# Optimization experiments

Measured on AMD Instinct MI355X. Metric: run time of the kernel, lower is better.

## Reference

```python
import jax, jax.numpy as jnp
import numpy as np

D = 256; FF = 1024; NH = 8; NL = 4; NP = 4; DH = D // NH
SHAPES = [(64, 64), (32, 32), (16, 16), (8, 8)]
B = 4; N = sum(h * w for h, w in SHAPES)


def _ln(x, g, b, eps=1e-5):
    m = jnp.mean(x, -1, keepdims=True)
    v = jnp.var(x, -1, keepdims=True)
    return (x - m) * jax.lax.rsqrt(v + eps) * g + b


def _bilinear(v, x, y, H, W):
    # v: [B, H*W, nh, dh]; x, y: [B, Nq, nh, P] pixel coords (grid_sample, align_corners=False, zero pad)
    x0 = jnp.floor(x); y0 = jnp.floor(y)
    fx = x - x0; fy = y - y0
    x0 = x0.astype(jnp.int32); y0 = y0.astype(jnp.int32)
    dh = v.shape[-1]
    acc = 0.0
    for xi, yi, w in ((x0, y0, (1 - fx) * (1 - fy)),
                      (x0 + 1, y0, fx * (1 - fy)),
                      (x0, y0 + 1, (1 - fx) * fy),
                      (x0 + 1, y0 + 1, fx * fy)):
        valid = ((xi >= 0) & (xi < W) & (yi >= 0) & (yi < H)).astype(v.dtype)
        idx = jnp.clip(yi, 0, H - 1) * W + jnp.clip(xi, 0, W - 1)  # [B,Nq,nh,P]
        Bq, Nq, nh, P = idx.shape
        idx2 = idx.transpose(0, 1, 3, 2).reshape(Bq, Nq * P, nh, 1)
        idx2 = jnp.broadcast_to(idx2, (Bq, Nq * P, nh, dh))
        g = jnp.take_along_axis(v, idx2, axis=1)  # [B, Nq*P, nh, dh]
        g = g.reshape(Bq, Nq, P, nh, dh).transpose(0, 1, 3, 2, 4)  # [B,Nq,nh,P,dh]
        acc = acc + g * (w * valid)[..., None]
    return acc


def _msdeform(value, loc, attn, shapes):
    # value [B,N,nh,dh]; loc [B,Nq,nh,L,P,2] in [0,1]; attn [B,Nq,nh,L,P]
    out = 0.0; start = 0
    for l, (H, W) in enumerate(shapes):
        v = value[:, start:start + H * W]
        start += H * W
        x = loc[:, :, :, l, :, 0] * W - 0.5
        y = loc[:, :, :, l, :, 1] * H - 0.5
        s = _bilinear(v, x, y, H, W)  # [B,Nq,nh,P,dh]
        out = out + jnp.einsum('bqhpd,bqhp->bqhd', s, attn[:, :, :, l, :])
    return out


def _forward(src, pos, reference_points, w_value, b_value, w_off, b_off, w_attn, b_attn,
             w_out, b_out, g1, be1, w1, b1, w2, b2, g2, be2, padding_mask, shapes):
    q = src + pos
    value = src @ w_value.T + b_value
    value = jnp.where(padding_mask[..., None], 0.0, value).reshape(B, N, NH, DH)
    off = (q @ w_off.T + b_off).reshape(B, N, NH, NL, NP, 2)
    attn = jax.nn.softmax((q @ w_attn.T + b_attn).reshape(B, N, NH, NL * NP), axis=-1)
    attn = attn.reshape(B, N, NH, NL, NP)
    normalizer = jnp.array([[w, h] for h, w in shapes], jnp.float32)  # [L,2] as (W,H)
    loc = reference_points[:, :, None, :, None, :] + off / normalizer[None, None, None, :, None, :]
    a = _msdeform(value, loc, attn, shapes).reshape(B, N, D) @ w_out.T + b_out
    x = _ln(src + a, g1, be1)
    f = jax.nn.relu(x @ w1.T + b1) @ w2.T + b2
    return _ln(x + f, g2, be2)


def setup_inputs() -> dict:
    key = jax.random.key(0)
    ks = iter(jax.random.split(key, 24))
    def p(shape, scale=0.02):
        return jax.random.normal(next(ks), shape, jnp.float32) * scale
    d = {}
    d['src'] = jax.random.normal(next(ks), (B, N, D), jnp.float32)
    d['pos'] = jax.random.normal(next(ks), (B, N, D), jnp.float32)
    d['reference_points'] = jax.random.uniform(next(ks), (B, N, NL, 2), dtype=jnp.float32)
    d['w_value'] = p((D, D)); d['b_value'] = jnp.zeros((D,), jnp.float32)
    d['w_off'] = p((NH * NL * NP * 2, D), 0.001); d['b_off'] = p((NH * NL * NP * 2,), 0.1)
    d['w_attn'] = p((NH * NL * NP, D)); d['b_attn'] = jnp.zeros((NH * NL * NP,), jnp.float32)
    d['w_out'] = p((D, D)); d['b_out'] = jnp.zeros((D,), jnp.float32)
    d['g1'] = jnp.ones((D,), jnp.float32); d['be1'] = jnp.zeros((D,), jnp.float32)
    d['w1'] = p((FF, D)); d['b1'] = jnp.zeros((FF,), jnp.float32)
    d['w2'] = p((D, FF)); d['b2'] = jnp.zeros((D,), jnp.float32)
    d['g2'] = jnp.ones((D,), jnp.float32); d['be2'] = jnp.zeros((D,), jnp.float32)
    d['spatial_shapes'] = jnp.array(SHAPES, jnp.int32)
    d['level_start_index'] = jnp.array(np.cumsum([0] + [h * w for h, w in SHAPES[:-1]]), jnp.int32)
    d['padding_mask'] = jnp.zeros((B, N), bool)
    return d


def reference(src, pos, reference_points, w_value, b_value, w_off, b_off, w_attn, b_attn,
              w_out, b_out, g1, be1, w1, b1, w2, b2, g2, be2,
              spatial_shapes, level_start_index, padding_mask):
    shapes = [tuple(map(int, s)) for s in np.asarray(spatial_shapes)]  # static per-level shapes
    return _forward(src, pos, reference_points, w_value, b_value, w_off, b_off, w_attn, b_attn,
                    w_out, b_out, g1, be1, w1, b1, w2, b2, g2, be2, padding_mask, shapes)
```

## Files before the change

### kernel.cpp

```cpp
#include <hip/hip_runtime.h>

#define B_SZ   4
#define NTOK   5440
#define MTOT   (B_SZ*NTOK)
#define DMODEL 256
#define FFDIM  1024

typedef __attribute__((ext_vector_type(8))) __bf16 bf16x8;
typedef __attribute__((ext_vector_type(4))) float  f32x4;

static __device__ __forceinline__ unsigned short f2b(float f) {
    unsigned u = __builtin_bit_cast(unsigned, f);
    u = (u + 0x7FFF + ((u >> 16) & 1)) >> 16;
    return (unsigned short)u;
}
static __device__ __forceinline__ float b2f(unsigned short s) {
    return __builtin_bit_cast(float, (unsigned)s << 16);
}
static __device__ __forceinline__ float lo_bf(unsigned u) {
    return __builtin_bit_cast(float, u << 16);
}
static __device__ __forceinline__ float hi_bf(unsigned u) {
    return __builtin_bit_cast(float, u & 0xffff0000u);
}

__global__ __launch_bounds__(256)
void mfma_gemm(const unsigned short* __restrict__ A,
               const unsigned short* __restrict__ Wt,
               const float* __restrict__ bias, const float* __restrict__ bias2,
               int bsplit,
               const unsigned char* __restrict__ rowmask,
               float* __restrict__ Cf, unsigned short* __restrict__ Cb,
               int M, int Nout, int K, int relu)
{
    __shared__ unsigned short As[128 * 32];
    __shared__ unsigned short Bs[128 * 32];
    const int tid  = threadIdx.x;
    const int lane = tid & 63;
    const int wave = tid >> 6;
    const int row0 = blockIdx.x * 128, col0 = blockIdx.y * 128;
    const int wr = (wave >> 1) * 64;
    const int wc = (wave & 1) * 64;
    const int mrow = lane & 15, quad = lane >> 4;

    f32x4 acc[4][4] = {};

    const int r0i = (0 * 256 + tid) >> 2, k0i = ((0 * 256 + tid) & 3) * 8;
    const int r1i = (1 * 256 + tid) >> 2, k1i = ((1 * 256 + tid) & 3) * 8;
    const int lds0 = (0 * 256 + wave * 64) * 8;
    const int lds1 = (1 * 256 + wave * 64) * 8;

    for (int k0 = 0; k0 < K; k0 += 32) {
        __syncthreads();
        {
            const unsigned short* ga0 = A  + (size_t)(row0 + r0i) * K + k0 + k0i;
            const unsigned short* gb0 = Wt + (size_t)(col0 + r0i) * K + k0 + k0i;
            const unsigned short* ga1 = A  + (size_t)(row0 + r1i) * K + k0 + k1i;
            const unsigned short* gb1 = Wt + (size_t)(col0 + r1i) * K + k0 + k1i;
            __builtin_amdgcn_global_load_lds((const __attribute__((address_space(1))) void*)ga0,
                                             (__attribute__((address_space(3))) void*)&As[lds0], 16, 0, 0);
            __builtin_amdgcn_global_load_lds((const __attribute__((address_space(1))) void*)gb0,
                                             (__attribute__((address_space(3))) void*)&Bs[lds0], 16, 0, 0);
            __builtin_amdgcn_global_load_lds((const __attribute__((address_space(1))) void*)ga1,
                                             (__attribute__((address_space(3))) void*)&As[lds1], 16, 0, 0);
            __builtin_amdgcn_global_load_lds((const __attribute__((address_space(1))) void*)gb1,
                                             (__attribute__((address_space(3))) void*)&Bs[lds1], 16, 0, 0);
        }
        __syncthreads();

        bf16x8 af[4], bfr[4];
        #pragma unroll
        for (int t4 = 0; t4 < 4; ++t4) {
            af[t4]  = *(const bf16x8*)&As[(wr + t4 * 16 + mrow) * 32 + quad * 8];
            bfr[t4] = *(const bf16x8*)&Bs[(wc + t4 * 16 + mrow) * 32 + quad * 8];
        }
        #pragma unroll
        for (int ti = 0; ti < 4; ++ti)
            #pragma unroll
            for (int tj = 0; tj < 4; ++tj)
                acc[ti][tj] = __builtin_amdgcn_mfma_f32_16x16x32_bf16(
                                  af[ti], bfr[tj], acc[ti][tj], 0, 0, 0);
    }

    #pragma unroll
    for (int tj = 0; tj < 4; ++tj) {
        const int col = col0 + wc + tj * 16 + mrow;
        const float bv = (col < bsplit) ? bias[col] : bias2[col - bsplit];
        #pragma unroll
        for (int ti = 0; ti < 4; ++ti) {
            #pragma unroll
            for (int r = 0; r < 4; ++r) {
                const int row = row0 + wr + ti * 16 + quad * 4 + r;
                float v = acc[ti][tj][r] + bv;
                if (relu) v = fmaxf(v, 0.f);
                if (rowmask && rowmask[row]) v = 0.f;
                if (Cf) Cf[(size_t)row * Nout + col] = v;
                else    Cb[(size_t)row * Nout + col] = f2b(v);
            }
        }
    }
}

__global__ __launch_bounds__(256)
void sampling_kernel(const unsigned short* __restrict__ value,
                     const unsigned short* __restrict__ oa,
                     const float* __restrict__ refp,
                     unsigned short* __restrict__ samp)
{
    __shared__ int4 s_pk[1024];
    const int t0  = blockIdx.x * 4;
    const int tid = threadIdx.x;

    #pragma unroll
    for (int rep = 0; rep < 2; ++rep) {
        const int e   = rep * 256 + tid;
        const int tok = e >> 7;
        const int hp  = e & 127;
        const int h   = hp >> 4, i16 = hp & 15, l = i16 >> 2;
        const int t   = t0 + tok;

        const float logit = b2f(oa[(size_t)t * 384 + 256 + h * 16 + i16]);
        float mx = logit;
        #pragma unroll
        for (int o = 8; o; o >>= 1) mx = fmaxf(mx, __shfl_xor(mx, o, 16));
        const float ex = __expf(logit - mx);
        float ssum = ex;
        #pragma unroll
        for (int o = 8; o; o >>= 1) ssum += __shfl_xor(ssum, o, 16);
        const float aw = ex / ssum;

        const int   Wl_t[4]   = {64, 32, 16, 8};
        const int   LSTB_t[4] = {0, 4096 * 512, 5120 * 512, 5376 * 512};
        const int   Wl   = Wl_t[l];
        const int   LSTB = LSTB_t[l];
        const float fW   = (float)Wl;

        const unsigned ov = *(const unsigned*)&oa[(size_t)t * 384 + h * 32 + i16 * 2];
        const float ox = lo_bf(ov), oy = hi_bf(ov);
        const float2 rxy = *(const float2*)&refp[(size_t)t * 8 + l * 2];
        const float x = rxy.x * fW + ox - 0.5f;
        const float y = rxy.y * fW + oy - 0.5f;
        const float x0 = floorf(x), y0 = floorf(y);
        const float fx = x - x0, fy = y - y0;
        const int   ix = (int)x0, iy = (int)y0;
        const bool  vx0 = (ix >= 0) & (ix < Wl), vx1 = (ix + 1 >= 0) & (ix + 1 < Wl);

        #pragma unroll
        for (int j = 0; j < 2; ++j) {
            const int  yv = iy + j;
            const bool vy = (yv >= 0) & (yv < Wl);
            const float wy = (j ? fy : 1.f - fy) * aw;
            const int  rowb = LSTB + yv * Wl * 512;
            const float w0 = (vy & vx0) ? wy * (1.f - fx) : 0.f;
            const float w1 = (vy & vx1) ? wy * fx : 0.f;
            const int  i0 = (vy & vx0) ? rowb + ix * 512 : 0;
            const int  i1 = (vy & vx1) ? rowb + (ix + 1) * 512 : 0;
            s_pk[e * 2 + j] = make_int4(i0, __float_as_int(w0), i1, __float_as_int(w1));
        }
    }
    __syncthreads();

    const int wv_  = tid >> 6;
    const int lane = tid & 63;
    const int h    = lane >> 3, dq = lane & 7;
    const int t    = t0 + wv_;
    const int b    = t / NTOK;
    const char* vb = (const char*)value + ((size_t)b * NTOK * 256 + h * 32 + dq * 4) * 2;
    const int4* pk = s_pk + (wv_ * 128 + h * 16) * 2;

    float a0 = 0.f, a1 = 0.f, a2 = 0.f, a3 = 0.f;
    #pragma unroll 8
    for (int i = 0; i < 32; ++i) {
        const int4 p = pk[i];
        const uint2 u0 = *(const uint2*)(vb + p.x);
        const uint2 u1 = *(const uint2*)(vb + p.z);
        const float w0 = __int_as_float(p.y), w1 = __int_as_float(p.w);
        a0 += lo_bf(u0.x) * w0; a1 += hi_bf(u0.x) * w0;
        a2 += lo_bf(u0.y) * w0; a3 += hi_bf(u0.y) * w0;
        a0 += lo_bf(u1.x) * w1; a1 += hi_bf(u1.x) * w1;
        a2 += lo_bf(u1.y) * w1; a3 += hi_bf(u1.y) * w1;
    }
    ushort4 o;
    o.x = f2b(a0); o.y = f2b(a1); o.z = f2b(a2); o.w = f2b(a3);
    *(ushort4*)(samp + (size_t)t * 256 + h * 32 + dq * 4) = o;
}

__global__ __launch_bounds__(256)
void ln_kernel(const float* __restrict__ resid, const float* __restrict__ y,
               const float* __restrict__ g, const float* __restrict__ be,
               float* __restrict__ out_f, unsigned short* __restrict__ out_b)
{
    const int wave = threadIdx.x >> 6;
    const int lane = threadIdx.x & 63;
    const int row  = blockIdx.x * 4 + wave;
    const size_t base = (size_t)row * 256 + (lane << 2);

    const float4 r = *(const float4*)(resid + base);
    float4 v       = *(const float4*)(y + base);
    v.x += r.x; v.y += r.y; v.z += r.z; v.w += r.w;

    float s  = v.x + v.y + v.z + v.w;
    float ss = v.x * v.x + v.y * v.y + v.z * v.z + v.w * v.w;
    #pragma unroll
    for (int off = 32; off; off >>= 1) {
        s  += __shfl_xor(s, off, 64);
        ss += __shfl_xor(ss, off, 64);
    }
    const float mean = s * (1.f / 256.f);
    const float var  = ss * (1.f / 256.f) - mean * mean;
    const float rstd = rsqrtf(var + 1e-5f);

    const float4 gv = *(const float4*)(g  + (lane << 2));
    const float4 bv = *(const float4*)(be + (lane << 2));
    float4 o;
    o.x = (v.x - mean) * rstd * gv.x + bv.x;
    o.y = (v.y - mean) * rstd * gv.y + bv.y;
    o.z = (v.z - mean) * rstd * gv.z + bv.z;
    o.w = (v.w - mean) * rstd * gv.w + bv.w;
    *(float4*)(out_f + base) = o;
    if (out_b) {
        ushort4 u; u.x = f2b(o.x); u.y = f2b(o.y); u.z = f2b(o.z); u.w = f2b(o.w);
        *(ushort4*)(out_b + base) = u;
    }
}

__global__ __launch_bounds__(256)
void prep_kernel(const float* __restrict__ src, const float* __restrict__ pos,
                 const float* __restrict__ wv, const float* __restrict__ woff,
                 const float* __restrict__ wattn, const float* __restrict__ wout,
                 const float* __restrict__ w1, const float* __restrict__ w2,
                 unsigned short* __restrict__ q_bf, unsigned short* __restrict__ src_bf,
                 unsigned short* __restrict__ wv_b, unsigned short* __restrict__ woa_b,
                 unsigned short* __restrict__ wout_b,
                 unsigned short* __restrict__ w1_b, unsigned short* __restrict__ w2_b)
{
    const int v = blockIdx.x * 256 + threadIdx.x;
    if (v < 1392640) {
        const float4 s = ((const float4*)src)[v];
        const float4 p = ((const float4*)pos)[v];
        ushort4 qo, so;
        qo.x = f2b(s.x + p.x); qo.y = f2b(s.y + p.y);
        qo.z = f2b(s.z + p.z); qo.w = f2b(s.w + p.w);
        so.x = f2b(s.x); so.y = f2b(s.y); so.z = f2b(s.z); so.w = f2b(s.w);
        ((ushort4*)q_bf)[v]   = qo;
        ((ushort4*)src_bf)[v] = so;
        return;
    }
    const int v2 = v - 1392640;
    const float* s; unsigned short* d; int off;
    if      (v2 <  16384) { s = wv;    d = wv_b;          off = v2; }
    else if (v2 <  32768) { s = woff;  d = woa_b;         off = v2 - 16384; }
    else if (v2 <  40960) { s = wattn; d = woa_b + 65536; off = v2 - 32768; }
    else if (v2 <  57344) { s = wout;  d = wout_b;        off = v2 - 40960; }
    else if (v2 < 122880) { s = w1;    d = w1_b;          off = v2 - 57344; }
    else                  { s = w2;    d = w2_b;          off = v2 - 122880; }
    const float4 f = ((const float4*)s)[off];
    ushort4 u; u.x = f2b(f.x); u.y = f2b(f.y); u.z = f2b(f.z); u.w = f2b(f.w);
    ((ushort4*)d)[off] = u;
}

extern "C" void kernel_launch(void* const* d_in, const int* in_sizes, int n_in,
                              void* d_out, int out_size, void* d_ws, size_t ws_size,
                              hipStream_t stream) {
    const float* src     = (const float*)d_in[0];
    const float* pos     = (const float*)d_in[1];
    const float* refp    = (const float*)d_in[2];
    const float* w_value = (const float*)d_in[3];
    const float* b_value = (const float*)d_in[4];
    const float* w_off   = (const float*)d_in[5];
    const float* b_off   = (const float*)d_in[6];
    const float* w_attn  = (const float*)d_in[7];
    const float* b_attn  = (const float*)d_in[8];
    const float* w_out   = (const float*)d_in[9];
    const float* b_out   = (const float*)d_in[10];
    const float* g1      = (const float*)d_in[11];
    const float* be1     = (const float*)d_in[12];
    const float* w1      = (const float*)d_in[13];
    const float* b1      = (const float*)d_in[14];
    const float* w2      = (const float*)d_in[15];
    const float* b2      = (const float*)d_in[16];
    const float* g2      = (const float*)d_in[17];
    const float* be2     = (const float*)d_in[18];
    const unsigned char* pmask = (const unsigned char*)d_in[21];

    char* ws = (char*)d_ws;
    const size_t SZ16 = (size_t)MTOT * 256 * 2;
    unsigned short* q_bf    = (unsigned short*)(ws);
    unsigned short* src_bf  = (unsigned short*)(ws + SZ16);
    float*          aout    = (float*)(ws);
    float*          f       = (float*)(ws);
    unsigned short* value_b = (unsigned short*)(ws + 2 * SZ16);
    unsigned short* oa_b    = (unsigned short*)(ws + 3 * SZ16);
    float*          x       = (float*)(ws + 2 * SZ16);
    unsigned short* samp    = (unsigned short*)(ws + 50135040ULL);
    unsigned short* x_bf    = (unsigned short*)(ws + 50135040ULL);
    unsigned short* h_bf    = (unsigned short*)(ws + 61276160ULL);
    unsigned short* wts     = (unsigned short*)(ws + 105840640ULL);
    unsigned short* wv_b    = wts;
    unsigned short* woa_b   = wv_b   + 65536;
    unsigned short* wout_b  = woa_b  + 98304;
    unsigned short* w1_b    = wout_b + 65536;
    unsigned short* w2_b    = w1_b   + 262144;

    const dim3 blk(256);

    prep_kernel<<<dim3(6176), blk, 0, stream>>>(src, pos, w_value, w_off, w_attn,
                                                w_out, w1, w2, q_bf, src_bf,
                                                wv_b, woa_b, wout_b, w1_b, w2_b);
    mfma_gemm<<<dim3(MTOT / 128, 2), blk, 0, stream>>>(
        src_bf, wv_b, b_value, b_value, DMODEL, pmask, nullptr, value_b,
        MTOT, DMODEL, DMODEL, 0);
    mfma_gemm<<<dim3(MTOT / 128, 3), blk, 0, stream>>>(
        q_bf, woa_b, b_off, b_attn, DMODEL, nullptr, nullptr, oa_b,
        MTOT, 384, DMODEL, 0);
    sampling_kernel<<<dim3(MTOT / 4), blk, 0, stream>>>(value_b, oa_b, refp, samp);
    mfma_gemm<<<dim3(MTOT / 128, 2), blk, 0, stream>>>(
        samp, wout_b, b_out, b_out, DMODEL, nullptr, aout, nullptr,
        MTOT, DMODEL, DMODEL, 0);
    ln_kernel<<<dim3(MTOT / 4), blk, 0, stream>>>(src, aout, g1, be1, x, x_bf);
    mfma_gemm<<<dim3(MTOT / 128, FFDIM / 128), blk, 0, stream>>>(
        x_bf, w1_b, b1, b1, FFDIM, nullptr, nullptr, h_bf, MTOT, FFDIM, DMODEL, 1);
    mfma_gemm<<<dim3(MTOT / 128, 2), blk, 0, stream>>>(
        h_bf, w2_b, b2, b2, DMODEL, nullptr, f, nullptr, MTOT, DMODEL, FFDIM, 0);
    ln_kernel<<<dim3(MTOT / 4), blk, 0, stream>>>(x, f, g2, be2, (float*)d_out, nullptr);
}
```

Measured before the change: 318.9 us.

## Fuse value/offset GEMMs, fuse LayerNorm into output GEMMs, pad sampling LDS

The separate value and offset/attention projection GEMMs are merged into a single launch that chooses its operands per block column. The output-projection and FFN2 GEMMs now use full-row 64x256 tiles and apply bias, residual add and LayerNorm in the epilogue, which removes both standalone LN kernels and the fp32 intermediate round trips. The sampling kernel's shared-memory packet array is padded to a stride of 33 per head to reduce bank conflicts. The workspace layout is rearranged to match. The trade-off is that the LN-fused GEMMs launch fewer, taller blocks (340) and each block loads the whole 256-column weight slice.

```diff
diff --git a/kernel.cpp b/kernel.cpp
--- a/kernel.cpp
+++ b/kernel.cpp
@@ -24,13 +24,86 @@
     return __builtin_bit_cast(float, u & 0xffff0000u);
 }
 
+#define GLL(gp, lp) __builtin_amdgcn_global_load_lds( \
+    (const __attribute__((address_space(1))) void*)(gp), \
+    (__attribute__((address_space(3))) void*)(lp), 16, 0, 0)
+
+__global__ __launch_bounds__(256)
+void qkv_gemm(const unsigned short* __restrict__ src_bf,
+              const unsigned short* __restrict__ q_bf,
+              const unsigned short* __restrict__ wv_b,
+              const unsigned short* __restrict__ woa_b,
+              const float* __restrict__ b_value,
+              const float* __restrict__ b_off, const float* __restrict__ b_attn,
+              const unsigned char* __restrict__ rowmask,
+              unsigned short* __restrict__ value_b, unsigned short* __restrict__ oa_b)
+{
+    const int K = 256;
+    const int y = blockIdx.y;
+    const bool isv = (y < 2);
+    const unsigned short* A  = isv ? src_bf : q_bf;
+    const unsigned short* Wt = isv ? wv_b : woa_b;
+    unsigned short* C = isv ? value_b : oa_b;
+    const int ldc  = isv ? 256 : 384;
+    const int col0 = (isv ? y : (y - 2)) * 128;
+
+    __shared__ unsigned short As[128 * 32];
+    __shared__ unsigned short Bs[128 * 32];
+    const int tid  = threadIdx.x;
+    const int lane = tid & 63;
+    const int wave = tid >> 6;
+    const int row0 = blockIdx.x * 128;
+    const int wr = (wave >> 1) * 64, wc = (wave & 1) * 64;
+    const int mrow = lane & 15, quad = lane >> 4;
+
+    f32x4 acc[4][4] = {};
+    const int ri0 = tid >> 2,            ki0 = (tid & 3) * 8;
+    const int ri1 = (256 + tid) >> 2,    ki1 = ((256 + tid) & 3) * 8;
+    const int lds0 = (wave * 64) * 8, lds1 = (256 + wave * 64) * 8;
+
+    for (int k0 = 0; k0 < K; k0 += 32) {
+        __syncthreads();
+        GLL(A  + (size_t)(row0 + ri0) * K + k0 + ki0, &As[lds0]);
+        GLL(Wt + (size_t)(col0 + ri0) * K + k0 + ki0, &Bs[lds0]);
+        GLL(A  + (size_t)(row0 + ri1) * K + k0 + ki1, &As[lds1]);
+        GLL(Wt + (size_t)(col0 + ri1) * K + k0 + ki1, &Bs[lds1]);
+        __syncthreads();
+
+        bf16x8 af[4], bfr[4];
+        #pragma unroll
+        for (int t4 = 0; t4 < 4; ++t4) {
+            af[t4]  = *(const bf16x8*)&As[(wr + t4 * 16 + mrow) * 32 + quad * 8];
+            bfr[t4] = *(const bf16x8*)&Bs[(wc + t4 * 16 + mrow) * 32 + quad * 8];
+        }
+        #pragma unroll
+        for (int ti = 0; ti < 4; ++ti)
+            #pragma unroll
+            for (int tj = 0; tj < 4; ++tj)
+                acc[ti][tj] = __builtin_amdgcn_mfma_f32_16x16x32_bf16(
+                                  af[ti], bfr[tj], acc[ti][tj], 0, 0, 0);
+    }
+
+    #pragma unroll
+    for (int tj = 0; tj < 4; ++tj) {
+        const int col = col0 + wc + tj * 16 + mrow;
+        const float bv = isv ? b_value[col] : (col < 256 ? b_off[col] : b_attn[col - 256]);
+        #pragma unroll
+        for (int ti = 0; ti < 4; ++ti)
+            #pragma unroll
+            for (int r = 0; r < 4; ++r) {
+                const int row = row0 + wr + ti * 16 + quad * 4 + r;
+                float v = acc[ti][tj][r] + bv;
+                if (isv && rowmask[row]) v = 0.f;
+                C[(size_t)row * ldc + col] = f2b(v);
+            }
+    }
+}
+
 __global__ __launch_bounds__(256)
 void mfma_gemm(const unsigned short* __restrict__ A,
                const unsigned short* __restrict__ Wt,
-               const float* __restrict__ bias, const float* __restrict__ bias2,
-               int bsplit,
-               const unsigned char* __restrict__ rowmask,
-               float* __restrict__ Cf, unsigned short* __restrict__ Cb,
+               const float* __restrict__ bias,
+               unsigned short* __restrict__ Cb,
                int M, int Nout, int K, int relu)
 {
     __shared__ unsigned short As[128 * 32];
@@ -39,33 +112,20 @@
     const int lane = tid & 63;
     const int wave = tid >> 6;
     const int row0 = blockIdx.x * 128, col0 = blockIdx.y * 128;
-    const int wr = (wave >> 1) * 64;
-    const int wc = (wave & 1) * 64;
+    const int wr = (wave >> 1) * 64, wc = (wave & 1) * 64;
     const int mrow = lane & 15, quad = lane >> 4;
 
     f32x4 acc[4][4] = {};
-
-    const int r0i = (0 * 256 + tid) >> 2, k0i = ((0 * 256 + tid) & 3) * 8;
-    const int r1i = (1 * 256 + tid) >> 2, k1i = ((1 * 256 + tid) & 3) * 8;
-    const int lds0 = (0 * 256 + wave * 64) * 8;
-    const int lds1 = (1 * 256 + wave * 64) * 8;
+    const int ri0 = tid >> 2,            ki0 = (tid & 3) * 8;
+    const int ri1 = (256 + tid) >> 2,    ki1 = ((256 + tid) & 3) * 8;
+    const int lds0 = (wave * 64) * 8, lds1 = (256 + wave * 64) * 8;
 
     for (int k0 = 0; k0 < K; k0 += 32) {
         __syncthreads();
-        {
-            const unsigned short* ga0 = A  + (size_t)(row0 + r0i) * K + k0 + k0i;
-            const unsigned short* gb0 = Wt + (size_t)(col0 + r0i) * K + k0 + k0i;
-            const unsigned short* ga1 = A  + (size_t)(row0 + r1i) * K + k0 + k1i;
-            const unsigned short* gb1 = Wt + (size_t)(col0 + r1i) * K + k0 + k1i;
-            __builtin_amdgcn_global_load_lds((const __attribute__((address_space(1))) void*)ga0,
-                                             (__attribute__((address_space(3))) void*)&As[lds0], 16, 0, 0);
-            __builtin_amdgcn_global_load_lds((const __attribute__((address_space(1))) void*)gb0,
-                                             (__attribute__((address_space(3))) void*)&Bs[lds0], 16, 0, 0);
-            __builtin_amdgcn_global_load_lds((const __attribute__((address_space(1))) void*)ga1,
-                                             (__attribute__((address_space(3))) void*)&As[lds1], 16, 0, 0);
-            __builtin_amdgcn_global_load_lds((const __attribute__((address_space(1))) void*)gb1,
-                                             (__attribute__((address_space(3))) void*)&Bs[lds1], 16, 0, 0);
-        }
+        GLL(A  + (size_t)(row0 + ri0) * K + k0 + ki0, &As[lds0]);
+        GLL(Wt + (size_t)(col0 + ri0) * K + k0 + ki0, &Bs[lds0]);
+        GLL(A  + (size_t)(row0 + ri1) * K + k0 + ki1, &As[lds1]);
+        GLL(Wt + (size_t)(col0 + ri1) * K + k0 + ki1, &Bs[lds1]);
         __syncthreads();
 
         bf16x8 af[4], bfr[4];
@@ -85,17 +145,114 @@
     #pragma unroll
     for (int tj = 0; tj < 4; ++tj) {
         const int col = col0 + wc + tj * 16 + mrow;
-        const float bv = (col < bsplit) ? bias[col] : bias2[col - bsplit];
-        #pragma unroll
-        for (int ti = 0; ti < 4; ++ti) {
+        const float bv = bias[col];
+        #pragma unroll
+        for (int ti = 0; ti < 4; ++ti)
             #pragma unroll
             for (int r = 0; r < 4; ++r) {
                 const int row = row0 + wr + ti * 16 + quad * 4 + r;
                 float v = acc[ti][tj][r] + bv;
                 if (relu) v = fmaxf(v, 0.f);
-                if (rowmask && rowmask[row]) v = 0.f;
-                if (Cf) Cf[(size_t)row * Nout + col] = v;
-                else    Cb[(size_t)row * Nout + col] = f2b(v);
+                Cb[(size_t)row * Nout + col] = f2b(v);
+            }
+    }
+}
+
+__global__ __launch_bounds__(256)
+void gemm_ln(const unsigned short* __restrict__ A,
+             const unsigned short* __restrict__ Wt,
+             const float* __restrict__ bias,
+             const float* __restrict__ resid,
+             const float* __restrict__ g, const float* __restrict__ be,
+             float* __restrict__ out_f, unsigned short* __restrict__ out_b,
+             int K)
+{
+    __shared__ unsigned short As[64 * 32];
+    __shared__ unsigned short Bs[256 * 32];
+    __shared__ float s_red[64][8];
+
+    const int tid  = threadIdx.x;
+    const int lane = tid & 63;
+    const int wave = tid >> 6;
+    const int row0 = blockIdx.x * 64;
+    const int mrow = lane & 15, quad = lane >> 4;
+    const int colw = wave * 64;
+
+    f32x4 acc[4][4] = {};
+    const int ri = tid >> 2, ki = (tid & 3) * 8;
+
+    for (int k0 = 0; k0 < K; k0 += 32) {
+        __syncthreads();
+        GLL(A + (size_t)(row0 + ri) * K + k0 + ki, &As[(wave * 64) * 8]);
+        #pragma unroll
+        for (int i = 0; i < 4; ++i)
+            GLL(Wt + (size_t)(i * 64 + ri) * K + k0 + ki, &Bs[(i * 256 + wave * 64) * 8]);
+        __syncthreads();
+
+        bf16x8 af[4], bfr[4];
+        #pragma unroll
+        for (int t4 = 0; t4 < 4; ++t4) {
+            af[t4]  = *(const bf16x8*)&As[(t4 * 16 + mrow) * 32 + quad * 8];
+            bfr[t4] = *(const bf16x8*)&Bs[(colw + t4 * 16 + mrow) * 32 + quad * 8];
+        }
+        #pragma unroll
+        for (int ti = 0; ti < 4; ++ti)
+            #pragma unroll
+            for (int tj = 0; tj < 4; ++tj)
+                acc[ti][tj] = __builtin_amdgcn_mfma_f32_16x16x32_bf16(
+                                  af[ti], bfr[tj], acc[ti][tj], 0, 0, 0);
+    }
+
+    float bv[4], gv[4], bev[4];
+    #pragma unroll
+    for (int tj = 0; tj < 4; ++tj) {
+        const int col = colw + tj * 16 + mrow;
+        bv[tj] = bias[col]; gv[tj] = g[col]; bev[tj] = be[col];
+    }
+
+    __syncthreads();
+
+    #pragma unroll
+    for (int ti = 0; ti < 4; ++ti) {
+        #pragma unroll
+        for (int r = 0; r < 4; ++r) {
+            const int row_local = ti * 16 + quad * 4 + r;
+            const int row = row0 + row_local;
+            float s = 0.f, sq = 0.f;
+            #pragma unroll
+            for (int tj = 0; tj < 4; ++tj) {
+                const int col = colw + tj * 16 + mrow;
+                float t = acc[ti][tj][r] + bv[tj] + resid[(size_t)row * 256 + col];
+                acc[ti][tj][r] = t;
+                s += t; sq += t * t;
+            }
+            #pragma unroll
+            for (int m = 1; m < 16; m <<= 1) {
+                s  += __shfl_xor(s, m, 64);
+                sq += __shfl_xor(sq, m, 64);
+            }
+            if (mrow == 0) { s_red[row_local][wave] = s; s_red[row_local][4 + wave] = sq; }
+        }
+    }
+    __syncthreads();
+
+    #pragma unroll
+    for (int ti = 0; ti < 4; ++ti) {
+        #pragma unroll
+        for (int r = 0; r < 4; ++r) {
+            const int row_local = ti * 16 + quad * 4 + r;
+            const int row = row0 + row_local;
+            const float4 su = *(const float4*)&s_red[row_local][0];
+            const float4 qu = *(const float4*)&s_red[row_local][4];
+            const float mean = (su.x + su.y + su.z + su.w) * (1.f / 256.f);
+            const float var  = (qu.x + qu.y + qu.z + qu.w) * (1.f / 256.f) - mean * mean;
+            const float rstd = rsqrtf(var + 1e-5f);
+            #pragma unroll
+            for (int tj = 0; tj < 4; ++tj) {
+                const int col = colw + tj * 16 + mrow;
+                const float o = (acc[ti][tj][r] - mean) * rstd * gv[tj] + bev[tj];
+                out_f[(size_t)row * 256 + col] = o;
+                if (out_b) out_b[(size_t)row * 256 + col] = f2b(o);
             }
         }
     }
@@ -107,7 +264,7 @@
                      const float* __restrict__ refp,
                      unsigned short* __restrict__ samp)
 {
-    __shared__ int4 s_pk[1024];
+    __shared__ int4 s_pk[4 * 264];
     const int t0  = blockIdx.x * 4;
     const int tid = threadIdx.x;
 
@@ -155,7 +312,8 @@
             const float w1 = (vy & vx1) ? wy * fx : 0.f;
             const int  i0 = (vy & vx0) ? rowb + ix * 512 : 0;
             const int  i1 = (vy & vx1) ? rowb + (ix + 1) * 512 : 0;
-            s_pk[e * 2 + j] = make_int4(i0, __float_as_int(w0), i1, __float_as_int(w1));
+            s_pk[tok * 264 + h * 33 + i16 * 2 + j] =
+                make_int4(i0, __float_as_int(w0), i1, __float_as_int(w1));
         }
     }
     __syncthreads();
@@ -166,7 +324,7 @@
     const int t    = t0 + wv_;
     const int b    = t / NTOK;
     const char* vb = (const char*)value + ((size_t)b * NTOK * 256 + h * 32 + dq * 4) * 2;
-    const int4* pk = s_pk + (wv_ * 128 + h * 16) * 2;
+    const int4* pk = s_pk + wv_ * 264 + h * 33;
 
     float a0 = 0.f, a1 = 0.f, a2 = 0.f, a3 = 0.f;
     #pragma unroll 8
@@ -183,45 +341,6 @@
     ushort4 o;
     o.x = f2b(a0); o.y = f2b(a1); o.z = f2b(a2); o.w = f2b(a3);
     *(ushort4*)(samp + (size_t)t * 256 + h * 32 + dq * 4) = o;
-}
-
-__global__ __launch_bounds__(256)
-void ln_kernel(const float* __restrict__ resid, const float* __restrict__ y,
-               const float* __restrict__ g, const float* __restrict__ be,
-               float* __restrict__ out_f, unsigned short* __restrict__ out_b)
-{
-    const int wave = threadIdx.x >> 6;
-    const int lane = threadIdx.x & 63;
-    const int row  = blockIdx.x * 4 + wave;
-    const size_t base = (size_t)row * 256 + (lane << 2);
-
-    const float4 r = *(const float4*)(resid + base);
-    float4 v       = *(const float4*)(y + base);
-    v.x += r.x; v.y += r.y; v.z += r.z; v.w += r.w;
-
-    float s  = v.x + v.y + v.z + v.w;
-    float ss = v.x * v.x + v.y * v.y + v.z * v.z + v.w * v.w;
-    #pragma unroll
-    for (int off = 32; off; off >>= 1) {
-        s  += __shfl_xor(s, off, 64);
-        ss += __shfl_xor(ss, off, 64);
-    }
-    const float mean = s * (1.f / 256.f);
-    const float var  = ss * (1.f / 256.f) - mean * mean;
-    const float rstd = rsqrtf(var + 1e-5f);
-
-    const float4 gv = *(const float4*)(g  + (lane << 2));
-    const float4 bv = *(const float4*)(be + (lane << 2));
-    float4 o;
-    o.x = (v.x - mean) * rstd * gv.x + bv.x;
-    o.y = (v.y - mean) * rstd * gv.y + bv.y;
-    o.z = (v.z - mean) * rstd * gv.z + bv.z;
-    o.w = (v.w - mean) * rstd * gv.w + bv.w;
-    *(float4*)(out_f + base) = o;
-    if (out_b) {
-        ushort4 u; u.x = f2b(o.x); u.y = f2b(o.y); u.z = f2b(o.z); u.w = f2b(o.w);
-        *(ushort4*)(out_b + base) = u;
-    }
 }
 
 __global__ __launch_bounds__(256)
@@ -287,15 +406,14 @@
     const size_t SZ16 = (size_t)MTOT * 256 * 2;
     unsigned short* q_bf    = (unsigned short*)(ws);
     unsigned short* src_bf  = (unsigned short*)(ws + SZ16);
-    float*          aout    = (float*)(ws);
-    float*          f       = (float*)(ws);
     unsigned short* value_b = (unsigned short*)(ws + 2 * SZ16);
     unsigned short* oa_b    = (unsigned short*)(ws + 3 * SZ16);
-    float*          x       = (float*)(ws + 2 * SZ16);
-    unsigned short* samp    = (unsigned short*)(ws + 50135040ULL);
-    unsigned short* x_bf    = (unsigned short*)(ws + 50135040ULL);
-    unsigned short* h_bf    = (unsigned short*)(ws + 61276160ULL);
-    unsigned short* wts     = (unsigned short*)(ws + 105840640ULL);
+    unsigned short* samp    = (unsigned short*)(ws + 3 * SZ16 + SZ16 * 3 / 2);
+    unsigned short* h_bf    = (unsigned short*)(ws + 5 * SZ16 + SZ16 * 3 / 2);
+    unsigned short* wts     = (unsigned short*)(ws + 9 * SZ16 + SZ16 * 3 / 2);
+    float*          x       = (float*)(ws);
+    unsigned short* x_bf    = (unsigned short*)(ws + 2 * SZ16);
+
     unsigned short* wv_b    = wts;
     unsigned short* woa_b   = wv_b   + 65536;
     unsigned short* wout_b  = woa_b  + 98304;
@@ -307,20 +425,13 @@
     prep_kernel<<<dim3(6176), blk, 0, stream>>>(src, pos, w_value, w_off, w_attn,
                                                 w_out, w1, w2, q_bf, src_bf,
                                                 wv_b, woa_b, wout_b, w1_b, w2_b);
-    mfma_gemm<<<dim3(MTOT / 128, 2), blk, 0, stream>>>(
-        src_bf, wv_b, b_value, b_value, DMODEL, pmask, nullptr, value_b,
-        MTOT, DMODEL, DMODEL, 0);
-    mfma_gemm<<<dim3(MTOT / 128, 3), blk, 0, stream>>>(
-        q_bf, woa_b, b_off, b_attn, DMODEL, nullptr, nullptr, oa_b,
-        MTOT, 384, DMODEL, 0);
+    qkv_gemm<<<dim3(MTOT / 128, 5), blk, 0, stream>>>(
+        src_bf, q_bf, wv_b, woa_b, b_value, b_off, b_attn, pmask, value_b, oa_b);
     sampling_kernel<<<dim3(MTOT / 4), blk, 0, stream>>>(value_b, oa_b, refp, samp);
-    mfma_gemm<<<dim3(MTOT / 128, 2), blk, 0, stream>>>(
-        samp, wout_b, b_out, b_out, DMODEL, nullptr, aout, nullptr,
-        MTOT, DMODEL, DMODEL, 0);
-    ln_kernel<<<dim3(MTOT / 4), blk, 0, stream>>>(src, aout, g1, be1, x, x_bf);
+    gemm_ln<<<dim3(MTOT / 64), blk, 0, stream>>>(
+        samp, wout_b, b_out, src, g1, be1, x, x_bf, DMODEL);
     mfma_gemm<<<dim3(MTOT / 128, FFDIM / 128), blk, 0, stream>>>(
-        x_bf, w1_b, b1, b1, FFDIM, nullptr, nullptr, h_bf, MTOT, FFDIM, DMODEL, 1);
-    mfma_gemm<<<dim3(MTOT / 128, 2), blk, 0, stream>>>(
-        h_bf, w2_b, b2, b2, DMODEL, nullptr, f, nullptr, MTOT, DMODEL, FFDIM, 0);
-    ln_kernel<<<dim3(MTOT / 4), blk, 0, stream>>>(x, f, g2, be2, (float*)d_out, nullptr);
-}
+        x_bf, w1_b, b1, h_bf, MTOT, FFDIM, DMODEL, 1);
+    gemm_ln<<<dim3(MTOT / 64), blk, 0, stream>>>(
+        h_bf, w2_b, b2, x, g2, be2, (float*)d_out, nullptr, FFDIM);
+}
```

New measurement: 292.9 us. -8.2%, faster.
